# Performance work log

Measured on AMD Instinct MI355X. Metric: run time of the kernel, lower is better.

The kernel has to match this reference:

```python
import jax, jax.numpy as jnp
import numpy as np
from jax import lax

B, T, I, H = 128, 48, 128, 512


def setup_inputs() -> dict:
    key = jax.random.key(0)
    ks = jax.random.split(key, 16)
    s = lambda *sh: 1.0 / np.sqrt(sh[-1])
    inp = {
        "decoder_x": jax.random.normal(ks[0], (B, T, I), jnp.float32),
        "x": jax.random.normal(ks[1], (B, T, 3), jnp.float32),
        # xavier_normal for [num_layers=1, B, H] -> std = sqrt(2/(B+H))
        "h0": jax.random.normal(ks[2], (B, H), jnp.float32) * np.sqrt(2.0 / (B + H)),
        "W1": jax.random.normal(ks[3], (H, H), jnp.float32) * s(H),
        "b1": jnp.zeros((H,), jnp.float32),
        "W2": jax.random.normal(ks[4], (H, I), jnp.float32) * s(I),
        "b2": jnp.zeros((H,), jnp.float32),
        "W3": jax.random.normal(ks[5], (1, H), jnp.float32) * s(H),
        "b3": jnp.zeros((1,), jnp.float32),
        "W4": jax.random.normal(ks[6], (H, I + 3), jnp.float32) * s(I + 3),
        "b4": jnp.zeros((H,), jnp.float32),
        "W_ih": jax.random.normal(ks[7], (3 * H, H), jnp.float32) * s(H),
        "W_hh": jax.random.normal(ks[8], (3 * H, H), jnp.float32) * s(H),
        "b_ih": jnp.zeros((3 * H,), jnp.float32),
        "b_hh": jnp.zeros((3 * H,), jnp.float32),
        "Wfc": jax.random.normal(ks[9], (1, H), jnp.float32) * s(H),
        "bfc": jnp.zeros((1,), jnp.float32),
    }
    return inp


def reference(decoder_x, x, h0, W1, b1, W2, b2, W3, b3, W4, b4,
              W_ih, W_hh, b_ih, b_hh, Wfc, bfc):
    Bc, Tc, Ic = decoder_x.shape
    # layer2(decoder_x) is step-invariant: compute once. [B, T, H]
    w2 = jnp.einsum('bti,hi->bth', decoder_x, W2) + b2

    def step(carry, x_t):
        h, _ = carry  # h: [B, H]
        w1 = h @ W1.T + b1                              # [B, H]
        # attention energies over the T_1 encoder window
        e = jnp.tanh(w1[:, None, :] + w2) @ W3[0] + b3[0]   # [B, T]
        a = jax.nn.softmax(e, axis=1)                   # [B, T]
        c = jnp.einsum('bti,bt->bi', decoder_x, a)      # weighted context [B, I]
        y0 = jnp.concatenate([c, x_t], axis=1) @ W4.T + b4  # [B, H]
        # single-step GRU (PyTorch gate order r, z, n)
        gi = y0 @ W_ih.T + b_ih
        gh = h @ W_hh.T + b_hh
        ir, iz, in_ = jnp.split(gi, 3, axis=1)
        hr, hz, hn = jnp.split(gh, 3, axis=1)
        r = jax.nn.sigmoid(ir + hr)
        z = jax.nn.sigmoid(iz + hz)
        n = jnp.tanh(in_ + r * hn)
        h_new = (1.0 - z) * n + z * h
        return (h_new, a), None

    xs = jnp.swapaxes(x, 0, 1)  # [T, B, 3]
    (h_f, a_f), _ = lax.scan(step, (h0, jnp.zeros((Bc, Tc), decoder_x.dtype)), xs)
    re = h_f @ Wfc.T + bfc      # fc(final_output[:, -1, :])  -> [B, 1]
    return re, a_f[:, :, None]  # weighted_alpha from last step [B, T, 1]
```

## Files before the change

kernel.cpp:

```cpp
#include <hip/hip_runtime.h>


typedef _Float16 half8 __attribute__((ext_vector_type(8)));
typedef _Float16 h2v  __attribute__((ext_vector_type(2)));
typedef float    f32x4 __attribute__((ext_vector_type(4)));
typedef unsigned int u32x3 __attribute__((ext_vector_type(3)));

#define OFF_BAR   0u
#define OFF_BZ    32768u
#define OFF_BC    40960u
#define OFF_WZ    65536u
#define OFF_WCT   2162688u
#define OFF_W2H   3178496u
#define OFF_HGH   9732096u
#define OFF_ZG    9863168u
#define OFF_DW    10911744u

__device__ __forceinline__ float fexp2(float x) { return __builtin_amdgcn_exp2f(x); }
__device__ __forceinline__ float frcp(float x)  { return __builtin_amdgcn_rcpf(x); }
__device__ __forceinline__ float fast_tanh(float x) {
  x = fminf(fmaxf(x, -15.f), 15.f);
  float e = fexp2(x * 2.8853900817779268f);
  return (e - 1.f) * frcp(e + 1.f);
}
__device__ __forceinline__ float fast_sigmoid(float x) {
  x = fminf(fmaxf(x, -30.f), 30.f);
  float e = fexp2(x * 1.4426950408889634f);
  return e * frcp(e + 1.f);
}

__device__ __forceinline__ void st_u32(unsigned int* p, unsigned int v) {
  __hip_atomic_store(p, v, __ATOMIC_RELAXED, __HIP_MEMORY_SCOPE_AGENT);
}
union H4 { unsigned long long u; _Float16 h[4]; };
union HU { unsigned int u; h2v h; };

__device__ __forceinline__ f32x4 ld16_sc(const void* p) {
  f32x4 v;
  asm volatile("global_load_dwordx4 %0, %1, off sc0 sc1\n\t"
               "s_waitcnt vmcnt(0)"
               : "=v"(v) : "v"(p) : "memory");
  return v;
}
__device__ __forceinline__ void ld16x2_sc(const void* p0, const void* p1,
                                          f32x4* a, f32x4* b) {
  asm volatile("global_load_dwordx4 %0, %2, off sc0 sc1\n\t"
               "global_load_dwordx4 %1, %3, off sc0 sc1\n\t"
               "s_waitcnt vmcnt(0)"
               : "=v"(*a), "=v"(*b) : "v"(p0), "v"(p1) : "memory");
}
__device__ __forceinline__ void st16_sc(void* p, f32x4 v) {
  asm volatile("global_store_dwordx4 %0, %1, off sc0 sc1"
               :: "v"(p), "v"(v) : "memory");
}
__device__ __forceinline__ void drain_vm() {
  asm volatile("s_waitcnt vmcnt(0)" ::: "memory");
  __builtin_amdgcn_sched_barrier(0);
}

__device__ __forceinline__ void poll_ge(unsigned int* fp, bool active,
                                        unsigned int target) {
  for (;;) {
    unsigned int v = active
      ? __hip_atomic_load(fp, __ATOMIC_RELAXED, __HIP_MEMORY_SCOPE_AGENT)
      : target;
    if (__ballot(v < target) == 0) break;
    __builtin_amdgcn_s_sleep(1);
  }
  __asm__ __volatile__("" ::: "memory");
}

__global__ __launch_bounds__(256) void prep_all(
    const float* __restrict__ dx, const float* __restrict__ h0,
    const float* __restrict__ W1, const float* __restrict__ Whh,
    const float* __restrict__ b1, const float* __restrict__ bhh,
    const float* __restrict__ Wih, const float* __restrict__ W4,
    const float* __restrict__ b4, const float* __restrict__ bih,
    const float* __restrict__ W2, const float* __restrict__ b2,
    _Float16* __restrict__ hgh,
    _Float16* __restrict__ Wzh, float* __restrict__ bz,
    float* __restrict__ bc, _Float16* __restrict__ WcT,
    _Float16* __restrict__ w2h, unsigned int* __restrict__ bar)
{
  __shared__ __align__(16) char smem[58368];
  const int bid = blockIdx.x;
  const int tid = threadIdx.x;
  const int lane = tid & 63, wv = tid >> 6;

  if (bid == 0) {
    for (int i = tid; i < 8192; i += 256) bar[i] = 0u;
  } else if (bid == 1) {
    for (int n = tid; n < 2048; n += 256)
      bz[n] = (n < 512) ? b1[n] : bhh[n - 512];
  } else if (bid < 18) {
    const int o0 = (bid - 2) * 96 + wv * 24;
    for (int it = 0; it < 24; ++it) {
      const int row = o0 + it;
      const float* r = Wih + row * 512 + lane * 8;
      float s = 0.f;
#pragma unroll
      for (int u = 0; u < 8; ++u) s += r[u] * b4[lane * 8 + u];
#pragma unroll
      for (int off = 32; off >= 1; off >>= 1) s += __shfl_xor(s, off);
      if (lane == 0) bc[row] = bih[row] + s;
    }
  } else if (bid < 34) {
    const int i0 = (bid - 18) * 4096 + tid * 16;
#pragma unroll
    for (int u = 0; u < 4; ++u) {
      float4 v = *(const float4*)(h0 + i0 + u * 4);
      H4 p; p.h[0] = (_Float16)v.x; p.h[1] = (_Float16)v.y;
      p.h[2] = (_Float16)v.z; p.h[3] = (_Float16)v.w;
      *(unsigned long long*)(hgh + i0 + u * 4) = p.u;
    }
  } else if (bid < 98) {
    const int i0 = (bid - 34) * 16384 + tid * 64;
#pragma unroll 4
    for (int u = 0; u < 16; ++u) {
      const int i = i0 + u * 4;
      const float* src = (i < 262144) ? (W1 + i) : (Whh + i - 262144);
      float4 v = *(const float4*)src;
      H4 p; p.h[0] = (_Float16)v.x; p.h[1] = (_Float16)v.y;
      p.h[2] = (_Float16)v.z; p.h[3] = (_Float16)v.w;
      *(unsigned long long*)(Wzh + i) = p.u;
    }
  } else if (bid < 194) {
    float* wih = (float*)smem;
    float* w4s = (float*)(smem + 4224);
    const int o0 = (bid - 98) * 16;
    const int k = tid;
    float acc[16];
#pragma unroll
    for (int i = 0; i < 16; ++i) acc[i] = 0.f;
    for (int jc = 0; jc < 512; jc += 64) {
      __syncthreads();
      for (int idx = tid; idx < 16 * 64; idx += 256) {
        int oo = idx >> 6, jj = idx & 63;
        wih[oo * 66 + jj] = Wih[(o0 + oo) * 512 + jc + jj];
      }
      for (int idx = tid; idx < 64 * 131; idx += 256) {
        int r = idx / 131, c = idx - r * 131;
        w4s[r * 132 + c] = W4[(jc + r) * 131 + c];
      }
      __syncthreads();
      if (k < 131) {
        for (int jj = 0; jj < 64; ++jj) {
          float w4v = w4s[jj * 132 + k];
#pragma unroll
          for (int oo = 0; oo < 16; ++oo) acc[oo] += wih[oo * 66 + jj] * w4v;
        }
      }
    }
    if (k < 131) {
#pragma unroll
      for (int oo = 0; oo < 16; ++oo)
        WcT[k * 1536 + o0 + oo] = (_Float16)acc[oo];
    }
  } else {
    float* dxa = (float*)smem;
    _Float16* w2t = (_Float16*)(smem + 24576);
    const int b = bid - 194;
    for (int idx = tid; idx < 48 * 128; idx += 256)
      dxa[idx] = dx[b * 6144 + idx];
    for (int hc = 0; hc < 4; ++hc) {
      __syncthreads();
      for (int idx = tid; idx < 128 * 128; idx += 256) {
        int hl = idx >> 7, i = idx & 127;
        w2t[i * 132 + hl] = (_Float16)W2[(hc * 128 + hl) * 128 + i];
      }
      __syncthreads();
      const int hh = tid & 127;
      const int tq = tid >> 7;
      const float b2v = b2[hc * 128 + hh];
      for (int tt = tq * 24; tt < tq * 24 + 24; ++tt) {
        float acc = b2v;
#pragma unroll 4
        for (int i = 0; i < 128; ++i)
          acc += dxa[tt * 128 + i] * (float)w2t[i * 132 + hh];
        w2h[(b * 48 + tt) * 512 + hc * 128 + hh] = (_Float16)acc;
      }
    }
  }
}

__global__ __launch_bounds__(256) void prep_dw(
    const float* __restrict__ dx, const _Float16* __restrict__ WcT,
    unsigned int* __restrict__ DW12)
{
  __shared__ float dxu[16 * 128];
  const int j = blockIdx.x;
  const int tid = threadIdx.x;
  const int u0 = j * 16;
  const float4* src = (const float4*)(dx + (size_t)u0 * 128);
  float4* dst4 = (float4*)dxu;
  for (int i = tid; i < 512; i += 256) dst4[i] = src[i];
  __syncthreads();
  const int c0 = tid * 2;
  float acc[16][6];
#pragma unroll
  for (int u = 0; u < 16; ++u)
#pragma unroll
    for (int g = 0; g < 6; ++g) acc[u][g] = 0.f;
  for (int k = 0; k < 128; ++k) {
    const _Float16* wr = WcT + k * 1536 + c0;
    h2v w0 = *(const h2v*)(wr);
    h2v w1v = *(const h2v*)(wr + 512);
    h2v w2v = *(const h2v*)(wr + 1024);
    const float f0 = (float)w0[0],  f1 = (float)w0[1];
    const float f2 = (float)w1v[0], f3 = (float)w1v[1];
    const float f4 = (float)w2v[0], f5 = (float)w2v[1];
#pragma unroll
    for (int u = 0; u < 16; ++u) {
      const float d = dxu[u * 128 + k];
      acc[u][0] += d * f0; acc[u][1] += d * f1; acc[u][2] += d * f2;
      acc[u][3] += d * f3; acc[u][4] += d * f4; acc[u][5] += d * f5;
    }
  }
#pragma unroll
  for (int u = 0; u < 16; ++u) {
    unsigned int* o = DW12 + (size_t)(u0 + u) * 768 + tid * 3;
    HU p;
    p.h[0] = (_Float16)acc[u][0]; p.h[1] = (_Float16)acc[u][1]; o[0] = p.u;
    p.h[0] = (_Float16)acc[u][2]; p.h[1] = (_Float16)acc[u][3]; o[1] = p.u;
    p.h[0] = (_Float16)acc[u][4]; p.h[1] = (_Float16)acc[u][5]; o[2] = p.u;
  }
}

#define DW_STEP(TB, CUR)                                                     \
  do {                                                                       \
    _Pragma("unroll")                                                        \
    for (int j = 0; j < 4; ++j) {                                            \
      const float a = asx[(TB) * 4 + j];                                     \
      HU p0, p1, p2; p0.u = CUR[j].x; p1.u = CUR[j].y; p2.u = CUR[j].z;      \
      aR0 += a * (float)p0.h[0]; aR1 += a * (float)p0.h[1];                  \
      aZ0 += a * (float)p1.h[0]; aZ1 += a * (float)p1.h[1];                  \
      aN0 += a * (float)p2.h[0]; aN1 += a * (float)p2.h[1];                  \
    }                                                                        \
    if ((TB) < 9) {                                                          \
      _Pragma("unroll")                                                      \
      for (int j = 0; j < 4; ++j)                                            \
        CUR[j] = *(const u32x3*)(dwp + (size_t)(((TB) + 3) * 4 + j) * 768);  \
    }                                                                        \
  } while (0)

__global__ __launch_bounds__(512, 1) void decoder_main(
    const float* __restrict__ xin, const float* __restrict__ h0,
    const float* __restrict__ W3, const float* __restrict__ b3,
    const float* __restrict__ Wfc, const float* __restrict__ bfc,
    const _Float16* __restrict__ Wzh, const float* __restrict__ bz,
    const _Float16* __restrict__ WcT, const float* __restrict__ bc,
    const _Float16* __restrict__ w2h, const unsigned int* __restrict__ DW12,
    _Float16* __restrict__ hgh, float* __restrict__ zg,
    unsigned int* __restrict__ bar, float* __restrict__ out)
{
  const int tid  = threadIdx.x;
  const int lane = tid & 63;
  const int wv   = tid >> 6;
  const int bid  = blockIdx.x;
  const int grp  = bid & 7;
  const int mem  = bid >> 3;
  const int b0   = grp * 16;
  const int myrow = b0 + mem;
  const int cb   = mem * 128;
  const int myIdx = grp * 16 + mem;
  const int base16 = grp * 16;
  unsigned int* zflag = bar;
  unsigned int* hflag = bar + 4096;

  __shared__ __align__(16) _Float16 w2lds[48 * 512];
  __shared__ __align__(16) char hlds[16384];
  __shared__ __align__(16) unsigned int dwlds[24 * 768];
  __shared__ __align__(16) float ztile[16 * 132];
  __shared__ __align__(16) float zrowlds[2048];
  __shared__ __align__(16) unsigned int hpack[256];
  __shared__ float xlds[48 * 4];
  __shared__ float es[48];
  __shared__ float asx[48];
  __shared__ float red[4];

  const int m = lane & 15, q = lane >> 4;

  half8 wzf[16];
  const int ncol = cb + wv * 16 + m;
  {
    const _Float16* wrow = Wzh + ncol * 512 + q * 8;
#pragma unroll
    for (int ks = 0; ks < 16; ++ks)
      wzf[ks] = *(const half8*)(wrow + ks * 32);
  }
  const float bzv = bz[ncol];
  float w3r[8];
#pragma unroll
  for (int u = 0; u < 8; ++u) w3r[u] = W3[lane * 8 + u];
  const float b3v  = b3[0];
  const float bfcv = bfc[0];

  const int t2 = tid & 255;
  const int c0 = t2 * 2;
  const float bcR0 = bc[c0],        bcR1 = bc[c0 + 1];
  const float bcZ0 = bc[512 + c0],  bcZ1 = bc[513 + c0];
  const float bcN0 = bc[1024 + c0], bcN1 = bc[1025 + c0];
  float wxR[3][2], wxZ[3][2], wxN[3][2];
#pragma unroll
  for (int j2 = 0; j2 < 3; ++j2) {
    const _Float16* wr = WcT + (128 + j2) * 1536 + c0;
    wxR[j2][0] = (float)wr[0];    wxR[j2][1] = (float)wr[1];
    wxZ[j2][0] = (float)wr[512];  wxZ[j2][1] = (float)wr[513];
    wxN[j2][0] = (float)wr[1024]; wxN[j2][1] = (float)wr[1025];
  }
  float hA = h0[myrow * 512 + c0];
  float hB = h0[myrow * 512 + c0 + 1];

  const float* __restrict__ zrow = zg + (size_t)myrow * 2048;
  const unsigned int* __restrict__ dwp =
      DW12 + (size_t)myrow * 48 * 768 + (size_t)t2 * 3;

  {
    const half8* w2src = (const half8*)(w2h + (size_t)myrow * 48 * 512);
    half8* w2dst = (half8*)w2lds;
    for (int i = tid; i < 3072; i += 512) w2dst[i] = w2src[i];
    for (int i = tid; i < 144; i += 512) {
      const int t = i / 3, j2 = i - t * 3;
      xlds[t * 4 + j2] = xin[myrow * 144 + i];
    }
    const unsigned int* dwsrc = DW12 + (size_t)myrow * 48 * 768;
    for (int i = tid; i < 24 * 256; i += 512) {
      u32x3 v = *(const u32x3*)(dwsrc + (size_t)i * 3);
      *(u32x3*)(dwlds + (size_t)i * 3) = v;
    }
  }
  __syncthreads();

  for (int step = 0; step < 48; ++step) {
    if (wv == 0)
      poll_ge(hflag + (size_t)(b0 + (lane & 15)) * 32, lane < 16,
              (unsigned int)step);
    __syncthreads();
    {
      const char* hb = (const char*)hgh + (size_t)b0 * 1024 + (size_t)tid * 16;
      f32x4 hv0, hv1;
      ld16x2_sc(hb, hb + 8192, &hv0, &hv1);
      const int n0 = tid, n1 = tid + 512;
      const int r0 = n0 >> 6, j0 = n0 & 63;
      const int r1 = n1 >> 6, j1 = n1 & 63;
      *(f32x4*)(hlds + r0 * 1024 + ((j0 * 16) ^ ((r0 & 7) << 4))) = hv0;
      *(f32x4*)(hlds + r1 * 1024 + ((j1 * 16) ^ ((r1 & 7) << 4))) = hv1;
    }
    __syncthreads();

    {
      half8 af[16];
      const char* hb = hlds + m * 1024;
      const int sw = (m & 7) << 4;
#pragma unroll
      for (int ks = 0; ks < 16; ++ks)
        af[ks] = *(const half8*)(hb + ((ks * 64 + q * 16) ^ sw));
      f32x4 acc = {bzv, bzv, bzv, bzv};
#pragma unroll
      for (int ks = 0; ks < 16; ++ks)
        acc = __builtin_amdgcn_mfma_f32_16x16x32_f16(af[ks], wzf[ks], acc, 0, 0, 0);
#pragma unroll
      for (int r = 0; r < 4; ++r)
        ztile[(q * 4 + r) * 132 + wv * 16 + m] = acc[r];
    }
    __syncthreads();
    {
      const int zr = tid >> 5, cq = tid & 31;
      f32x4 zv = *(const f32x4*)(ztile + zr * 132 + cq * 4);
      st16_sc(zg + (size_t)(b0 + zr) * 2048 + cb + cq * 4, zv);
    }
    drain_vm();
    __syncthreads();
    if (tid == 0) st_u32(&zflag[(size_t)myIdx * 32], (unsigned int)(step + 1));

    if (wv == 0)
      poll_ge(zflag + (size_t)(base16 + (lane & 15)) * 32, lane < 16,
              (unsigned int)(step + 1));
    __syncthreads();
    {
      f32x4 zv = ld16_sc((const char*)zrow + (size_t)tid * 16);
      *(f32x4*)(zrowlds + tid * 4) = zv;
    }
    __syncthreads();

    u32x3 bA[4], bB[4], bC[4];
    if (tid < 256) {
#pragma unroll
      for (int j = 0; j < 4; ++j) bA[j] = *(const u32x3*)(dwp + (size_t)(24 + j) * 768);
#pragma unroll
      for (int j = 0; j < 4; ++j) bB[j] = *(const u32x3*)(dwp + (size_t)(28 + j) * 768);
#pragma unroll
      for (int j = 0; j < 4; ++j) bC[j] = *(const u32x3*)(dwp + (size_t)(32 + j) * 768);
    }

    {
      float w1r[8];
#pragma unroll
      for (int u = 0; u < 8; ++u) w1r[u] = zrowlds[lane * 8 + u];
      for (int tt = 0; tt < 6; ++tt) {
        const int t = wv * 6 + tt;
        half8 w2v = *(const half8*)(w2lds + t * 512 + lane * 8);
        float p = 0.f;
#pragma unroll
        for (int u = 0; u < 8; ++u)
          p += w3r[u] * fast_tanh(w1r[u] + (float)w2v[u]);
#pragma unroll
        for (int off = 32; off >= 1; off >>= 1) p += __shfl_xor(p, off);
        if (lane == 0) es[t] = p + b3v;
      }
      __syncthreads();
      if (wv == 0) {
        float e = (lane < 48) ? es[lane] : -1e30f;
        float mx = e;
#pragma unroll
        for (int off = 32; off >= 1; off >>= 1) mx = fmaxf(mx, __shfl_xor(mx, off));
        float pe = (lane < 48) ? fexp2((e - mx) * 1.4426950408889634f) : 0.f;
        float s = pe;
#pragma unroll
        for (int off = 32; off >= 1; off >>= 1) s += __shfl_xor(s, off);
        float a = pe * frcp(s);
        if (lane < 48) {
          asx[lane] = a;
          if (step == 47) out[128 + myrow * 48 + lane] = a;
        }
      }
      __syncthreads();
    }

    if (tid < 256) {
      float aR0 = bcR0, aR1 = bcR1, aZ0 = bcZ0, aZ1 = bcZ1, aN0 = bcN0, aN1 = bcN1;
#pragma unroll 4
      for (int t = 0; t < 24; ++t) {
        const float a = asx[t];
        u32x3 d = *(const u32x3*)(dwlds + (size_t)(t * 256 + t2) * 3);
        HU p0, p1, p2; p0.u = d.x; p1.u = d.y; p2.u = d.z;
        aR0 += a * (float)p0.h[0]; aR1 += a * (float)p0.h[1];
        aZ0 += a * (float)p1.h[0]; aZ1 += a * (float)p1.h[1];
        aN0 += a * (float)p2.h[0]; aN1 += a * (float)p2.h[1];
      }
      DW_STEP(6, bA);  DW_STEP(7, bB);  DW_STEP(8, bC);
      DW_STEP(9, bA);  DW_STEP(10, bB); DW_STEP(11, bC);

      const float x0 = xlds[step * 4], x1 = xlds[step * 4 + 1], x2 = xlds[step * 4 + 2];
      aR0 += x0 * wxR[0][0] + x1 * wxR[1][0] + x2 * wxR[2][0];
      aR1 += x0 * wxR[0][1] + x1 * wxR[1][1] + x2 * wxR[2][1];
      aZ0 += x0 * wxZ[0][0] + x1 * wxZ[1][0] + x2 * wxZ[2][0];
      aZ1 += x0 * wxZ[0][1] + x1 * wxZ[1][1] + x2 * wxZ[2][1];
      aN0 += x0 * wxN[0][0] + x1 * wxN[1][0] + x2 * wxN[2][0];
      aN1 += x0 * wxN[0][1] + x1 * wxN[1][1] + x2 * wxN[2][1];

      const float2 gR = *(const float2*)(zrowlds + 512 + c0);
      const float2 gZ = *(const float2*)(zrowlds + 1024 + c0);
      const float2 gN = *(const float2*)(zrowlds + 1536 + c0);
      const float r0 = fast_sigmoid(aR0 + gR.x), r1 = fast_sigmoid(aR1 + gR.y);
      const float z0 = fast_sigmoid(aZ0 + gZ.x), z1 = fast_sigmoid(aZ1 + gZ.y);
      const float n0 = fast_tanh(aN0 + r0 * gN.x), n1 = fast_tanh(aN1 + r1 * gN.y);
      hA = (1.f - z0) * n0 + z0 * hA;
      hB = (1.f - z1) * n1 + z1 * hB;
      HU hp; hp.h[0] = (_Float16)hA; hp.h[1] = (_Float16)hB;
      hpack[t2] = hp.u;
    }
    __syncthreads();
    if (tid < 64) {
      f32x4 hv = *(const f32x4*)((const char*)hpack + tid * 16);
      st16_sc((char*)hgh + (size_t)myrow * 1024 + (size_t)tid * 16, hv);
    }
    drain_vm();
    if (tid == 0) st_u32(&hflag[(size_t)myrow * 32], (unsigned int)(step + 1));
  }

  if (tid < 256) {
    float p = hA * Wfc[c0] + hB * Wfc[c0 + 1];
#pragma unroll
    for (int off = 32; off >= 1; off >>= 1) p += __shfl_xor(p, off);
    if (lane == 0) red[wv] = p;
  }
  __syncthreads();
  if (tid == 0) out[myrow] = red[0] + red[1] + red[2] + red[3] + bfcv;
}

extern "C" void kernel_launch(void* const* d_in, const int* in_sizes, int n_in,
                              void* d_out, int out_size, void* d_ws, size_t ws_size,
                              hipStream_t stream) {
  (void)in_sizes; (void)n_in; (void)out_size; (void)ws_size;
  const float* dx  = (const float*)d_in[0];
  const float* xin = (const float*)d_in[1];
  const float* h0  = (const float*)d_in[2];
  const float* W1  = (const float*)d_in[3];
  const float* b1  = (const float*)d_in[4];
  const float* W2  = (const float*)d_in[5];
  const float* b2  = (const float*)d_in[6];
  const float* W3  = (const float*)d_in[7];
  const float* b3  = (const float*)d_in[8];
  const float* W4  = (const float*)d_in[9];
  const float* b4  = (const float*)d_in[10];
  const float* Wih = (const float*)d_in[11];
  const float* Whh = (const float*)d_in[12];
  const float* bih = (const float*)d_in[13];
  const float* bhh = (const float*)d_in[14];
  const float* Wfc = (const float*)d_in[15];
  const float* bfc = (const float*)d_in[16];

  char* ws = (char*)d_ws;
  unsigned int* bar = (unsigned int*)(ws + OFF_BAR);
  float*     bz  = (float*)(ws + OFF_BZ);
  float*     bc  = (float*)(ws + OFF_BC);
  _Float16*  Wzh = (_Float16*)(ws + OFF_WZ);
  _Float16*  WcT = (_Float16*)(ws + OFF_WCT);
  _Float16*  w2h = (_Float16*)(ws + OFF_W2H);
  _Float16*  hgh = (_Float16*)(ws + OFF_HGH);
  float*     zg  = (float*)(ws + OFF_ZG);
  unsigned int* DW12 = (unsigned int*)(ws + OFF_DW);

  prep_all<<<322, 256, 0, stream>>>(dx, h0, W1, Whh, b1, bhh, Wih, W4, b4, bih,
                                    W2, b2, hgh, Wzh, bz, bc, WcT, w2h, bar);
  prep_dw<<<384, 256, 0, stream>>>(dx, WcT, DW12);
  decoder_main<<<128, 512, 0, stream>>>(xin, h0, W3, b3, Wfc, bfc,
                                        Wzh, bz, WcT, bc, w2h, DW12,
                                        hgh, zg, bar, (float*)d_out);
}
```

Measured before the change: 853.2 us.

## Replace z-flag barrier with sentinel-valued data polling on the gate buffer

Instead of each block draining stores, setting a per-block flag, and polling 16 flags before reading the shared z/gate row, the consumer now polls the data itself. It spins until no element equals a NaN sentinel, then rewrites the sentinel so the next step can detect fresh data. The prep kernel gains 16 extra blocks to fill zg with the sentinel beforehand. This removes one drain plus a flag round-trip per step, at the cost of polling on the full data footprint. Correctness relies on 16-byte stores being observed atomically and on the sentinel reset never racing with the next step's writes.

```diff
diff --git a/kernel.cpp b/kernel.cpp
--- a/kernel.cpp
+++ b/kernel.cpp
@@ -5,6 +5,8 @@
 typedef _Float16 h2v  __attribute__((ext_vector_type(2)));
 typedef float    f32x4 __attribute__((ext_vector_type(4)));
 typedef unsigned int u32x3 __attribute__((ext_vector_type(3)));
+
+#define SENT_U 0xFFC00000u
 
 #define OFF_BAR   0u
 #define OFF_BZ    32768u
@@ -80,7 +82,8 @@
     _Float16* __restrict__ hgh,
     _Float16* __restrict__ Wzh, float* __restrict__ bz,
     float* __restrict__ bc, _Float16* __restrict__ WcT,
-    _Float16* __restrict__ w2h, unsigned int* __restrict__ bar)
+    _Float16* __restrict__ w2h, unsigned int* __restrict__ bar,
+    float* __restrict__ zg)
 {
   __shared__ __align__(16) char smem[58368];
   const int bid = blockIdx.x;
@@ -156,7 +159,7 @@
       for (int oo = 0; oo < 16; ++oo)
         WcT[k * 1536 + o0 + oo] = (_Float16)acc[oo];
     }
-  } else {
+  } else if (bid < 322) {
     float* dxa = (float*)smem;
     _Float16* w2t = (_Float16*)(smem + 24576);
     const int b = bid - 194;
@@ -180,6 +183,11 @@
         w2h[(b * 48 + tt) * 512 + hc * 128 + hh] = (_Float16)acc;
       }
     }
+  } else {
+    float4 s4;
+    s4.x = s4.y = s4.z = s4.w = __uint_as_float(SENT_U);
+    float4* dst = (float4*)zg + (size_t)(bid - 322) * 4096;
+    for (int i = tid; i < 4096; i += 256) dst[i] = s4;
   }
 }
 
@@ -262,9 +270,6 @@
   const int b0   = grp * 16;
   const int myrow = b0 + mem;
   const int cb   = mem * 128;
-  const int myIdx = grp * 16 + mem;
-  const int base16 = grp * 16;
-  unsigned int* zflag = bar;
   unsigned int* hflag = bar + 4096;
 
   __shared__ __align__(16) _Float16 w2lds[48 * 512];
@@ -369,17 +374,24 @@
       f32x4 zv = *(const f32x4*)(ztile + zr * 132 + cq * 4);
       st16_sc(zg + (size_t)(b0 + zr) * 2048 + cb + cq * 4, zv);
     }
-    drain_vm();
-    __syncthreads();
-    if (tid == 0) st_u32(&zflag[(size_t)myIdx * 32], (unsigned int)(step + 1));
-
-    if (wv == 0)
-      poll_ge(zflag + (size_t)(base16 + (lane & 15)) * 32, lane < 16,
-              (unsigned int)(step + 1));
-    __syncthreads();
+
     {
-      f32x4 zv = ld16_sc((const char*)zrow + (size_t)tid * 16);
+      const char* zsrc = (const char*)zrow + (size_t)tid * 16;
+      f32x4 zv = ld16_sc(zsrc);
+      for (;;) {
+        const bool stale =
+            (__float_as_uint(zv[0]) == SENT_U) |
+            (__float_as_uint(zv[1]) == SENT_U) |
+            (__float_as_uint(zv[2]) == SENT_U) |
+            (__float_as_uint(zv[3]) == SENT_U);
+        if (__ballot(stale) == 0ull) break;
+        __builtin_amdgcn_s_sleep(1);
+        if (stale) zv = ld16_sc(zsrc);
+      }
       *(f32x4*)(zrowlds + tid * 4) = zv;
+      f32x4 s4;
+      s4[0] = s4[1] = s4[2] = s4[3] = __uint_as_float(SENT_U);
+      st16_sc((void*)zsrc, s4);
     }
     __syncthreads();
 
@@ -466,6 +478,7 @@
       st16_sc((char*)hgh + (size_t)myrow * 1024 + (size_t)tid * 16, hv);
     }
     drain_vm();
+    __syncthreads();
     if (tid == 0) st_u32(&hflag[(size_t)myrow * 32], (unsigned int)(step + 1));
   }
 
@@ -512,8 +525,8 @@
   float*     zg  = (float*)(ws + OFF_ZG);
   unsigned int* DW12 = (unsigned int*)(ws + OFF_DW);
 
-  prep_all<<<322, 256, 0, stream>>>(dx, h0, W1, Whh, b1, bhh, Wih, W4, b4, bih,
-                                    W2, b2, hgh, Wzh, bz, bc, WcT, w2h, bar);
+  prep_all<<<338, 256, 0, stream>>>(dx, h0, W1, Whh, b1, bhh, Wih, W4, b4, bih,
+                                    W2, b2, hgh, Wzh, bz, bc, WcT, w2h, bar, zg);
   prep_dw<<<384, 256, 0, stream>>>(dx, WcT, DW12);
   decoder_main<<<128, 512, 0, stream>>>(xin, h0, W3, b3, Wfc, bfc,
                                         Wzh, bz, WcT, bc, w2h, DW12,
```

New measurement: 853.2 us. No clear change (+0.0%).
